# Kernel optimization log

Measured on AMD Instinct MI355X. Metric: run time of the kernel, lower is better.

Reference implementation:

```python
import jax, jax.numpy as jnp
import numpy as np

B, V, F = 64, 100000, 200000


def setup_inputs() -> dict:
    key = jax.random.key(0)
    k1, k2 = jax.random.split(key)
    verts = jax.random.normal(k1, (B, V, 3), dtype=jnp.float32)
    faces = jax.random.randint(k2, (F, 3), 0, V, dtype=jnp.int64)
    return {"verts": verts, "faces": faces}


def reference(verts, faces):
    # Directed edge list from triangles: each face (i,j,k) contributes
    # edges i<->j, j<->k, k<->i (with multiplicity), shape [6F].
    i, j, k = faces[:, 0], faces[:, 1], faces[:, 2]
    src = jnp.concatenate([i, j, j, k, k, i])
    dst = jnp.concatenate([j, i, k, j, i, k])

    nv = verts.shape[1]
    # Degree (neighbor count) per vertex; guard isolated vertices.
    deg = jnp.zeros((nv,), verts.dtype).at[src].add(1.0)
    deg = jnp.maximum(deg, 1.0)

    # Sum of neighbor positions via scatter-add: [B, V, 3]
    nbr_sum = jnp.zeros_like(verts).at[:, src].add(verts[:, dst])

    # Graph Laplacian: x - mean(neighbors)
    Lx = verts - nbr_sum / deg[None, :, None]

    # Per-vertex L2 norm, then mean over batch and vertices (scalar loss).
    per_vert = jnp.sqrt(jnp.sum(Lx * Lx, axis=-1))
    return per_vert.mean()
```

## Files before the change

kernel.cpp:

```cpp
#include <hip/hip_runtime.h>


#define BB 64
#define VV 100000
#define VP1 (VV + 1)
#define FF 200000
#define BUILD_BLOCKS ((FF + 255) / 256)
#define TR_BLOCKS ((VV + 31) / 32)
#define VBLK ((VV + 255) / 256)
#define NCHUNK (VV / 32)
#define SCALE 80.0f
#define BIAS_W ((512u) | (512u << 10) | (512u << 20))

typedef int iv4 __attribute__((ext_vector_type(4)));

#define WS_GHIST 400000u
#define WS_GCUR (400000u + 128u)
#define WS_VPERM (512u * 1024u)
#define WS_ADJC (2u * 1024u * 1024u)
#define WS_SLOTS (8u * 1024u * 1024u)
#define WS_T (21u * 1024u * 1024u)

__device__ __forceinline__ int quant10(float x) {
    int qi = (int)rintf(x * SCALE);
    qi = min(max(qi, -511), 511);
    return qi + 512;
}

__global__ __launch_bounds__(256) void build_kernel(
    const float* __restrict__ verts, const int* __restrict__ faces,
    int* __restrict__ count, int* __restrict__ ghist, int* __restrict__ slots,
    unsigned int* __restrict__ T10, float* __restrict__ out) {
    if (blockIdx.x < BUILD_BLOCKS) {
        __shared__ int h[17];
        if (threadIdx.x < 17) h[threadIdx.x] = 0;
        __syncthreads();
        int f = blockIdx.x * 256 + threadIdx.x;
        if (f == 0) out[0] = 0.0f;
        if (f < FF) {
            int i = faces[3 * f + 0];
            int j = faces[3 * f + 1];
            int k = faces[3 * f + 2];
            int pi = atomicAdd(count + i, 2);
            int pj = atomicAdd(count + j, 2);
            int pk = atomicAdd(count + k, 2);
            if (pi + 1 < 32) *(int2*)(slots + ((size_t)i << 5) + pi) = make_int2(j, k);
            if (pj + 1 < 32) *(int2*)(slots + ((size_t)j << 5) + pj) = make_int2(i, k);
            if (pk + 1 < 32) *(int2*)(slots + ((size_t)k << 5) + pk) = make_int2(i, j);
            { int uo = min(pi >> 1, 16), un = min((pi >> 1) + 1, 16);
              if (uo != un) { atomicSub(&h[uo], 1); atomicAdd(&h[un], 1); } }
            { int uo = min(pj >> 1, 16), un = min((pj >> 1) + 1, 16);
              if (uo != un) { atomicSub(&h[uo], 1); atomicAdd(&h[un], 1); } }
            { int uo = min(pk >> 1, 16), un = min((pk >> 1) + 1, 16);
              if (uo != un) { atomicSub(&h[uo], 1); atomicAdd(&h[un], 1); } }
        }
        __syncthreads();
        if (threadIdx.x < 17) {
            int d = h[threadIdx.x];
            if (blockIdx.x == 0 && threadIdx.x == 0) d += VV;
            if (d) atomicAdd(&ghist[threadIdx.x], d);
        }
    } else {
        __shared__ unsigned int lds32[64 * 52];
        int v0 = (blockIdx.x - BUILD_BLOCKS) * 32;
        if (blockIdx.x == BUILD_BLOCKS && threadIdx.x < 64) {
            int g = threadIdx.x >> 3, bp = threadIdx.x & 7;
            T10[((size_t)g * VP1 + VV) * 8 + bp] = BIAS_W;
        }
        #pragma unroll
        for (int it = 0; it < 6; ++it) {
            int idx = it * 256 + threadIdx.x;
            int b = idx / 24;
            int q = idx - b * 24;
            const float4 f4 =
                *(const float4*)(verts + (size_t)b * (VV * 3) + (size_t)v0 * 3 + 4 * q);
            unsigned int u0 = (unsigned)quant10(f4.x);
            unsigned int u1 = (unsigned)quant10(f4.y);
            unsigned int u2 = (unsigned)quant10(f4.z);
            unsigned int u3 = (unsigned)quant10(f4.w);
            uint2 d;
            d.x = u0 | (u1 << 16);
            d.y = u2 | (u3 << 16);
            *(uint2*)&lds32[b * 52 + 2 * q] = d;
        }
        __syncthreads();
        #pragma unroll
        for (int it = 0; it < 8; ++it) {
            int idx = it * 256 + threadIdx.x;
            int g = idx >> 8;
            int rem = idx & 255;
            int vloc = rem >> 3;
            int bp = rem & 7;
            int b = g * 8 + bp;
            int p0 = 3 * vloc;
            unsigned int dlo = lds32[b * 52 + (p0 >> 1)];
            unsigned int dhi = lds32[b * 52 + ((p0 + 2) >> 1)];
            unsigned long long pair = ((unsigned long long)dhi << 32) | dlo;
            pair >>= 16 * (p0 & 1);
            unsigned int u0 = (unsigned int)(pair & 1023u);
            unsigned int u1 = (unsigned int)((pair >> 16) & 1023u);
            unsigned int u2 = (unsigned int)((pair >> 32) & 1023u);
            T10[((size_t)g * VP1 + v0 + vloc) * 8 + bp] = u0 | (u1 << 10) | (u2 << 20);
        }
    }
}

__global__ __launch_bounds__(256) void scatter_kernel(
    const int* __restrict__ count, const int* __restrict__ ghist,
    int* __restrict__ gcurOff, const int* __restrict__ slots,
    uint2* __restrict__ vperm2, int* __restrict__ adjC) {
    __shared__ int h[17], base[17], sg[17];
    if (threadIdx.x < 17) {
        h[threadIdx.x] = 0;
        sg[threadIdx.x] = ghist[threadIdx.x];
    }
    __syncthreads();
    int v = blockIdx.x * 256 + threadIdx.x;
    int u = 0, lpos = 0, deg = 0;
    if (v < VV) {
        deg = count[v];
        u = min(deg, 32) >> 1;
        lpos = atomicAdd(&h[u], 1);
    }
    __syncthreads();
    if (threadIdx.x < 17 && h[threadIdx.x])
        base[threadIdx.x] = atomicAdd(&gcurOff[threadIdx.x], h[threadIdx.x]);
    __syncthreads();
    if (v < VV) {
        int pos = base[u] + lpos;
        int vstart = 0, astart = 0;
        for (int t = 0; t < u; ++t) {
            vstart += sg[t];
            astart += sg[t] * ((2 * t + 3) & ~3);
        }
        int use = 2 * u;
        int usep = (use + 3) & ~3;
        unsigned int aoff = (unsigned)(astart + pos * usep);
        uint2 e;
        e.x = (unsigned)v | ((unsigned)min(deg, 2047) << 20);
        e.y = aoff;
        vperm2[vstart + pos] = e;
        const int* src = slots + ((size_t)v << 5);
        int* dst = adjC + aoff;
        for (int t = 0; t < use; t += 2) *(int2*)(dst + t) = *(const int2*)(src + t);
    }
}

__inline__ __device__ float waveReduceSumF(float val) {
    #pragma unroll
    for (int o = 32; o > 0; o >>= 1) val += __shfl_down(val, o, 64);
    return val;
}

#define ACC(col, w)                            \
    {                                          \
        sx##col += (int)((w) & 1023u);         \
        sy##col += (int)(((w) >> 10) & 1023u); \
        sz##col += (int)((w) >> 20);           \
    }

#define LOSSC(col, w)                                         \
    {                                                         \
        float ax = (float)((int)((w) & 1023u) - 512);         \
        float ay = (float)((int)(((w) >> 10) & 1023u) - 512); \
        float az = (float)((int)((w) >> 20) - 512);           \
        float lx = ax - ((float)sx##col - corr) * invd;       \
        float ly = ay - ((float)sy##col - corr) * invd;       \
        float lz = az - ((float)sz##col - corr) * invd;       \
        acc += sqrtf(lx * lx + ly * ly + lz * lz);            \
    }

__global__ __launch_bounds__(256, 3) void loss_kernel(
    const unsigned int* __restrict__ T10, const uint2* __restrict__ vperm2,
    const int* __restrict__ adjC, float* __restrict__ out) {
    int lane = threadIdx.x & 63;
    int half = lane & 1;
    int ho = half << 2;
    int vg = lane >> 1;
    int g = blockIdx.x & 7;
    const unsigned int* Tg = T10 + (size_t)g * VP1 * 8;
    int wis = ((blockIdx.x >> 3) << 2) + (threadIdx.x >> 6);
    float acc = 0.f;
    #pragma unroll 1
    for (int k = 0; k < 3; ++k) {
        int c = wis + k * 1044;
        if (c >= NCHUNK) break;
        uint2 entry = vperm2[c * 32 + vg];
        int v = (int)(entry.x & 0xFFFFFu);
        int deg = (int)(entry.x >> 20);
        int use = min(deg, 32);
        int mu = __shfl(use, 62, 64);
        int mu8 = (mu + 7) & ~7;
        const int* row = adjC + entry.y;
        uint4 selfw = *(const uint4*)(Tg + ((size_t)v << 3) + ho);
        int sx0 = 0, sy0 = 0, sz0 = 0, sx1 = 0, sy1 = 0, sz1 = 0;
        int sx2 = 0, sy2 = 0, sz2 = 0, sx3 = 0, sy3 = 0, sz3 = 0;
        #pragma unroll 1
        for (int t = 0; t < mu8; t += 8) {
            iv4 pa = *(const iv4*)(row + t);
            iv4 pb = *(const iv4*)(row + t + 4);
            int n0 = (t < use) ? pa[0] : VV;
            int n1 = (t < use) ? pa[1] : VV;
            int n2 = (t + 2 < use) ? pa[2] : VV;
            int n3 = (t + 2 < use) ? pa[3] : VV;
            int n4 = (t + 4 < use) ? pb[0] : VV;
            int n5 = (t + 4 < use) ? pb[1] : VV;
            int n6 = (t + 6 < use) ? pb[2] : VV;
            int n7 = (t + 6 < use) ? pb[3] : VV;
            uint4 w0 = *(const uint4*)(Tg + ((size_t)n0 << 3) + ho);
            uint4 w1 = *(const uint4*)(Tg + ((size_t)n1 << 3) + ho);
            uint4 w2 = *(const uint4*)(Tg + ((size_t)n2 << 3) + ho);
            uint4 w3 = *(const uint4*)(Tg + ((size_t)n3 << 3) + ho);
            uint4 w4 = *(const uint4*)(Tg + ((size_t)n4 << 3) + ho);
            uint4 w5 = *(const uint4*)(Tg + ((size_t)n5 << 3) + ho);
            uint4 w6 = *(const uint4*)(Tg + ((size_t)n6 << 3) + ho);
            uint4 w7 = *(const uint4*)(Tg + ((size_t)n7 << 3) + ho);
            ACC(0, w0.x) ACC(1, w0.y) ACC(2, w0.z) ACC(3, w0.w)
            ACC(0, w1.x) ACC(1, w1.y) ACC(2, w1.z) ACC(3, w1.w)
            ACC(0, w2.x) ACC(1, w2.y) ACC(2, w2.z) ACC(3, w2.w)
            ACC(0, w3.x) ACC(1, w3.y) ACC(2, w3.z) ACC(3, w3.w)
            ACC(0, w4.x) ACC(1, w4.y) ACC(2, w4.z) ACC(3, w4.w)
            ACC(0, w5.x) ACC(1, w5.y) ACC(2, w5.z) ACC(3, w5.w)
            ACC(0, w6.x) ACC(1, w6.y) ACC(2, w6.z) ACC(3, w6.w)
            ACC(0, w7.x) ACC(1, w7.y) ACC(2, w7.z) ACC(3, w7.w)
        }
        float corr = 512.0f * (float)mu8;
        float invd = 1.0f / fmaxf((float)deg, 1.0f);
        LOSSC(0, selfw.x) LOSSC(1, selfw.y) LOSSC(2, selfw.z) LOSSC(3, selfw.w)
    }
    acc = waveReduceSumF(acc);
    __shared__ float wsums[4];
    int wid = threadIdx.x >> 6;
    if ((threadIdx.x & 63) == 0) wsums[wid] = acc;
    __syncthreads();
    if (threadIdx.x == 0) {
        float ssum = wsums[0] + wsums[1] + wsums[2] + wsums[3];
        atomicAdd(out, ssum * (1.0f / (SCALE * (float)BB * (float)VV)));
    }
}

extern "C" void kernel_launch(void* const* d_in, const int* in_sizes, int n_in,
                              void* d_out, int out_size, void* d_ws, size_t ws_size,
                              hipStream_t stream) {
    const float* verts = (const float*)d_in[0];
    const int* faces = (const int*)d_in[1];
    float* out = (float*)d_out;

    int* count = (int*)d_ws;
    int* ghist = (int*)((char*)d_ws + WS_GHIST);
    int* gcurOff = (int*)((char*)d_ws + WS_GCUR);
    uint2* vperm2 = (uint2*)((char*)d_ws + WS_VPERM);
    int* adjC = (int*)((char*)d_ws + WS_ADJC);
    int* slots = (int*)((char*)d_ws + WS_SLOTS);
    unsigned int* T10 = (unsigned int*)((char*)d_ws + WS_T);

    (void)hipMemsetAsync(d_ws, 0, WS_GCUR + 128u, stream);

    build_kernel<<<BUILD_BLOCKS + TR_BLOCKS, 256, 0, stream>>>(
        verts, faces, count, ghist, slots, T10, out);
    scatter_kernel<<<VBLK, 256, 0, stream>>>(count, ghist, gcurOff, slots, vperm2, adjC);

    loss_kernel<<<2088, 256, 0, stream>>>(T10, vperm2, adjC, out);
}
```

Before: 222.9 us.

## Interleave two vertex chunks per wave in loss kernel for more memory parallelism

Each wave of the loss kernel now handles two vertex chunks (A and B) at the same time. Their neighbor gathers are interleaved in one loop, so sixteen independent gathers are in flight per iteration. This replaces the previous serial loop over up to three chunks, and the grid grows from 2088 to 3136 blocks to fit the new split. The scatter copy also switches to 16-byte vector copies. The cost is roughly double the accumulator registers, which may lower occupancy, plus extra padded gathers when the two chunks have different max degrees.

```diff
diff --git a/kernel.cpp b/kernel.cpp
--- a/kernel.cpp
+++ b/kernel.cpp
@@ -9,6 +9,7 @@
 #define TR_BLOCKS ((VV + 31) / 32)
 #define VBLK ((VV + 255) / 256)
 #define NCHUNK (VV / 32)
+#define WIS2 1568
 #define SCALE 80.0f
 #define BIAS_W ((512u) | (512u << 10) | (512u << 20))
 
@@ -142,7 +143,7 @@
         vperm2[vstart + pos] = e;
         const int* src = slots + ((size_t)v << 5);
         int* dst = adjC + aoff;
-        for (int t = 0; t < use; t += 2) *(int2*)(dst + t) = *(const int2*)(src + t);
+        for (int t = 0; t < use; t += 4) *(iv4*)(dst + t) = *(const iv4*)(src + t);
     }
 }
 
@@ -159,7 +160,7 @@
         sz##col += (int)((w) >> 20);           \
     }
 
-#define LOSSC(col, w)                                         \
+#define LOSSC(col, w, corr, invd)                             \
     {                                                         \
         float ax = (float)((int)((w) & 1023u) - 512);         \
         float ay = (float)((int)(((w) >> 10) & 1023u) - 512); \
@@ -180,53 +181,96 @@
     int g = blockIdx.x & 7;
     const unsigned int* Tg = T10 + (size_t)g * VP1 * 8;
     int wis = ((blockIdx.x >> 3) << 2) + (threadIdx.x >> 6);
+    int cA = wis;
+    int cB = wis + WIS2;
+    bool bval = (cB < NCHUNK);
+    uint2 eA = vperm2[cA * 32 + vg];
+    uint2 eB = bval ? vperm2[cB * 32 + vg] : eA;
+    int vA = (int)(eA.x & 0xFFFFFu), degA = (int)(eA.x >> 20);
+    int vB = (int)(eB.x & 0xFFFFFu), degB = (int)(eB.x >> 20);
+    int useA = min(degA, 32);
+    int useB = bval ? min(degB, 32) : 0;
+    int m8A = (__shfl(useA, 62, 64) + 7) & ~7;
+    int m8B = (__shfl(useB, 62, 64) + 7) & ~7;
+    int tmax = max(m8A, m8B);
+    int tac = max(m8A - 8, 0), tbc = max(m8B - 8, 0);
+    const int* rowA = adjC + eA.y;
+    const int* rowB = adjC + eB.y;
+    uint4 selfwA = *(const uint4*)(Tg + ((size_t)vA << 3) + ho);
+    uint4 selfwB = *(const uint4*)(Tg + ((size_t)vB << 3) + ho);
+    int sxA0 = 0, syA0 = 0, szA0 = 0, sxA1 = 0, syA1 = 0, szA1 = 0;
+    int sxA2 = 0, syA2 = 0, szA2 = 0, sxA3 = 0, syA3 = 0, szA3 = 0;
+    int sxB0 = 0, syB0 = 0, szB0 = 0, sxB1 = 0, syB1 = 0, szB1 = 0;
+    int sxB2 = 0, syB2 = 0, szB2 = 0, sxB3 = 0, syB3 = 0, szB3 = 0;
     float acc = 0.f;
     #pragma unroll 1
-    for (int k = 0; k < 3; ++k) {
-        int c = wis + k * 1044;
-        if (c >= NCHUNK) break;
-        uint2 entry = vperm2[c * 32 + vg];
-        int v = (int)(entry.x & 0xFFFFFu);
-        int deg = (int)(entry.x >> 20);
-        int use = min(deg, 32);
-        int mu = __shfl(use, 62, 64);
-        int mu8 = (mu + 7) & ~7;
-        const int* row = adjC + entry.y;
-        uint4 selfw = *(const uint4*)(Tg + ((size_t)v << 3) + ho);
-        int sx0 = 0, sy0 = 0, sz0 = 0, sx1 = 0, sy1 = 0, sz1 = 0;
-        int sx2 = 0, sy2 = 0, sz2 = 0, sx3 = 0, sy3 = 0, sz3 = 0;
-        #pragma unroll 1
-        for (int t = 0; t < mu8; t += 8) {
-            iv4 pa = *(const iv4*)(row + t);
-            iv4 pb = *(const iv4*)(row + t + 4);
-            int n0 = (t < use) ? pa[0] : VV;
-            int n1 = (t < use) ? pa[1] : VV;
-            int n2 = (t + 2 < use) ? pa[2] : VV;
-            int n3 = (t + 2 < use) ? pa[3] : VV;
-            int n4 = (t + 4 < use) ? pb[0] : VV;
-            int n5 = (t + 4 < use) ? pb[1] : VV;
-            int n6 = (t + 6 < use) ? pb[2] : VV;
-            int n7 = (t + 6 < use) ? pb[3] : VV;
-            uint4 w0 = *(const uint4*)(Tg + ((size_t)n0 << 3) + ho);
-            uint4 w1 = *(const uint4*)(Tg + ((size_t)n1 << 3) + ho);
-            uint4 w2 = *(const uint4*)(Tg + ((size_t)n2 << 3) + ho);
-            uint4 w3 = *(const uint4*)(Tg + ((size_t)n3 << 3) + ho);
-            uint4 w4 = *(const uint4*)(Tg + ((size_t)n4 << 3) + ho);
-            uint4 w5 = *(const uint4*)(Tg + ((size_t)n5 << 3) + ho);
-            uint4 w6 = *(const uint4*)(Tg + ((size_t)n6 << 3) + ho);
-            uint4 w7 = *(const uint4*)(Tg + ((size_t)n7 << 3) + ho);
-            ACC(0, w0.x) ACC(1, w0.y) ACC(2, w0.z) ACC(3, w0.w)
-            ACC(0, w1.x) ACC(1, w1.y) ACC(2, w1.z) ACC(3, w1.w)
-            ACC(0, w2.x) ACC(1, w2.y) ACC(2, w2.z) ACC(3, w2.w)
-            ACC(0, w3.x) ACC(1, w3.y) ACC(2, w3.z) ACC(3, w3.w)
-            ACC(0, w4.x) ACC(1, w4.y) ACC(2, w4.z) ACC(3, w4.w)
-            ACC(0, w5.x) ACC(1, w5.y) ACC(2, w5.z) ACC(3, w5.w)
-            ACC(0, w6.x) ACC(1, w6.y) ACC(2, w6.z) ACC(3, w6.w)
-            ACC(0, w7.x) ACC(1, w7.y) ACC(2, w7.z) ACC(3, w7.w)
-        }
-        float corr = 512.0f * (float)mu8;
-        float invd = 1.0f / fmaxf((float)deg, 1.0f);
-        LOSSC(0, selfw.x) LOSSC(1, selfw.y) LOSSC(2, selfw.z) LOSSC(3, selfw.w)
+    for (int t = 0; t < tmax; t += 8) {
+        int ta = min(t, tac), tb = min(t, tbc);
+        iv4 paA = *(const iv4*)(rowA + ta);
+        iv4 pbA = *(const iv4*)(rowA + ta + 4);
+        iv4 paB = *(const iv4*)(rowB + tb);
+        iv4 pbB = *(const iv4*)(rowB + tb + 4);
+        int a0 = (t < useA) ? paA[0] : VV;
+        int a1 = (t < useA) ? paA[1] : VV;
+        int a2 = (t + 2 < useA) ? paA[2] : VV;
+        int a3 = (t + 2 < useA) ? paA[3] : VV;
+        int a4 = (t + 4 < useA) ? pbA[0] : VV;
+        int a5 = (t + 4 < useA) ? pbA[1] : VV;
+        int a6 = (t + 6 < useA) ? pbA[2] : VV;
+        int a7 = (t + 6 < useA) ? pbA[3] : VV;
+        int b0 = (t < useB) ? paB[0] : VV;
+        int b1 = (t < useB) ? paB[1] : VV;
+        int b2 = (t + 2 < useB) ? paB[2] : VV;
+        int b3 = (t + 2 < useB) ? paB[3] : VV;
+        int b4 = (t + 4 < useB) ? pbB[0] : VV;
+        int b5 = (t + 4 < useB) ? pbB[1] : VV;
+        int b6 = (t + 6 < useB) ? pbB[2] : VV;
+        int b7 = (t + 6 < useB) ? pbB[3] : VV;
+        uint4 wA0 = *(const uint4*)(Tg + ((size_t)a0 << 3) + ho);
+        uint4 wA1 = *(const uint4*)(Tg + ((size_t)a1 << 3) + ho);
+        uint4 wA2 = *(const uint4*)(Tg + ((size_t)a2 << 3) + ho);
+        uint4 wA3 = *(const uint4*)(Tg + ((size_t)a3 << 3) + ho);
+        uint4 wA4 = *(const uint4*)(Tg + ((size_t)a4 << 3) + ho);
+        uint4 wA5 = *(const uint4*)(Tg + ((size_t)a5 << 3) + ho);
+        uint4 wA6 = *(const uint4*)(Tg + ((size_t)a6 << 3) + ho);
+        uint4 wA7 = *(const uint4*)(Tg + ((size_t)a7 << 3) + ho);
+        uint4 wB0 = *(const uint4*)(Tg + ((size_t)b0 << 3) + ho);
+        uint4 wB1 = *(const uint4*)(Tg + ((size_t)b1 << 3) + ho);
+        uint4 wB2 = *(const uint4*)(Tg + ((size_t)b2 << 3) + ho);
+        uint4 wB3 = *(const uint4*)(Tg + ((size_t)b3 << 3) + ho);
+        uint4 wB4 = *(const uint4*)(Tg + ((size_t)b4 << 3) + ho);
+        uint4 wB5 = *(const uint4*)(Tg + ((size_t)b5 << 3) + ho);
+        uint4 wB6 = *(const uint4*)(Tg + ((size_t)b6 << 3) + ho);
+        uint4 wB7 = *(const uint4*)(Tg + ((size_t)b7 << 3) + ho);
+        ACC(A0, wA0.x) ACC(A1, wA0.y) ACC(A2, wA0.z) ACC(A3, wA0.w)
+        ACC(A0, wA1.x) ACC(A1, wA1.y) ACC(A2, wA1.z) ACC(A3, wA1.w)
+        ACC(A0, wA2.x) ACC(A1, wA2.y) ACC(A2, wA2.z) ACC(A3, wA2.w)
+        ACC(A0, wA3.x) ACC(A1, wA3.y) ACC(A2, wA3.z) ACC(A3, wA3.w)
+        ACC(A0, wA4.x) ACC(A1, wA4.y) ACC(A2, wA4.z) ACC(A3, wA4.w)
+        ACC(A0, wA5.x) ACC(A1, wA5.y) ACC(A2, wA5.z) ACC(A3, wA5.w)
+        ACC(A0, wA6.x) ACC(A1, wA6.y) ACC(A2, wA6.z) ACC(A3, wA6.w)
+        ACC(A0, wA7.x) ACC(A1, wA7.y) ACC(A2, wA7.z) ACC(A3, wA7.w)
+        ACC(B0, wB0.x) ACC(B1, wB0.y) ACC(B2, wB0.z) ACC(B3, wB0.w)
+        ACC(B0, wB1.x) ACC(B1, wB1.y) ACC(B2, wB1.z) ACC(B3, wB1.w)
+        ACC(B0, wB2.x) ACC(B1, wB2.y) ACC(B2, wB2.z) ACC(B3, wB2.w)
+        ACC(B0, wB3.x) ACC(B1, wB3.y) ACC(B2, wB3.z) ACC(B3, wB3.w)
+        ACC(B0, wB4.x) ACC(B1, wB4.y) ACC(B2, wB4.z) ACC(B3, wB4.w)
+        ACC(B0, wB5.x) ACC(B1, wB5.y) ACC(B2, wB5.z) ACC(B3, wB5.w)
+        ACC(B0, wB6.x) ACC(B1, wB6.y) ACC(B2, wB6.z) ACC(B3, wB6.w)
+        ACC(B0, wB7.x) ACC(B1, wB7.y) ACC(B2, wB7.z) ACC(B3, wB7.w)
+    }
+    float corr = 512.0f * (float)tmax;
+    float invdA = 1.0f / fmaxf((float)degA, 1.0f);
+    LOSSC(A0, selfwA.x, corr, invdA)
+    LOSSC(A1, selfwA.y, corr, invdA)
+    LOSSC(A2, selfwA.z, corr, invdA)
+    LOSSC(A3, selfwA.w, corr, invdA)
+    if (bval) {
+        float invdB = 1.0f / fmaxf((float)degB, 1.0f);
+        LOSSC(B0, selfwB.x, corr, invdB)
+        LOSSC(B1, selfwB.y, corr, invdB)
+        LOSSC(B2, selfwB.z, corr, invdB)
+        LOSSC(B3, selfwB.w, corr, invdB)
     }
     acc = waveReduceSumF(acc);
     __shared__ float wsums[4];
@@ -260,5 +304,5 @@
         verts, faces, count, ghist, slots, T10, out);
     scatter_kernel<<<VBLK, 256, 0, stream>>>(count, ghist, gcurOff, slots, vperm2, adjC);
 
-    loss_kernel<<<2088, 256, 0, stream>>>(T10, vperm2, adjC, out);
-}
+    loss_kernel<<<3136, 256, 0, stream>>>(T10, vperm2, adjC, out);
+}
```

After: 226.6 us. No clear change (+1.7%).
